# Kernel optimization log

Measured on AMD Instinct MI355X. Metric: run time of the kernel, lower is better.

The kernel has to match this reference:

```python
import jax, jax.numpy as jnp
import numpy as np

NUM_ITERS = 3  # num_iterations init arg


def squash(t, axis):
    # scale = ||t||^2 / (1+||t||^2); out = scale * t / ||t||
    sn = jnp.sum(t * t, axis=axis, keepdims=True)
    return (sn / (1.0 + sn)) * t / jnp.sqrt(sn)


def setup_inputs() -> dict:
    key = jax.random.key(0)
    k1, k2, k3 = jax.random.split(key, 3)
    B, I, O, DI, DO = 2048, 64, 32, 16, 16
    x = jax.random.normal(k1, (B, DI, I), dtype=jnp.float32)
    route_weights = jax.random.normal(k2, (O, I, DO, DI), dtype=jnp.float32)
    noise = 0.01 * jax.random.normal(k3, (O, I, DO, DI), dtype=jnp.float32)
    return {"x": x, "route_weights": route_weights, "noise": noise}


def reference(x, route_weights, noise):
    # random=True branch: perturbed routing weights
    W = route_weights + noise                      # [O,I,do,di]
    xt = jnp.transpose(x, (0, 2, 1))               # [B,I,di]
    # priors[b,o,i,d] = sum_e W[o,i,d,e] * xt[b,i,e]  (trailing singleton dim dropped)
    priors = jnp.einsum('oide,bie->boid', W, xt)   # [B,O,I,do]
    logits = jnp.zeros_like(priors)
    out = None
    for it in range(NUM_ITERS):
        probs = jax.nn.softmax(logits, axis=2)     # over input capsules I
        out = squash(jnp.sum(probs * priors, axis=2, keepdims=True), axis=3)  # [B,O,1,do]
        if it != NUM_ITERS - 1:
            logits = logits + priors * out         # routing-by-agreement update
    out = out[:, :, 0, :]                          # squeeze -> [B,O,do]
    # unsqueeze(0).transpose(2,1) -> [1,O,B,do]
    return jnp.transpose(out[None], (0, 2, 1, 3))
```

## Files before the change

kernel.cpp:

```cpp
#include <hip/hip_runtime.h>


#define THREADS 512

typedef __attribute__((ext_vector_type(2))) float f32x2;
typedef __attribute__((ext_vector_type(4))) float f32x4v;

__global__ __launch_bounds__(256) void wsum_kernel(
    const float* __restrict__ rw, const float* __restrict__ ns,
    float* __restrict__ w2)
{
    const int i = blockIdx.x * 256 + threadIdx.x;
    const float4 a = reinterpret_cast<const float4*>(rw)[i];
    const float4 n = reinterpret_cast<const float4*>(ns)[i];
    float4 r;
    r.x = a.x + n.x;  r.y = a.y + n.y;  r.z = a.z + n.z;  r.w = a.w + n.w;
    reinterpret_cast<float4*>(w2)[i] = r;
}

__device__ __forceinline__ void pk_fma(f32x2& acc, f32x2 a, f32x2 b) {
    asm("v_pk_fma_f32 %0, %1, %2, %0" : "+v"(acc) : "v"(a), "v"(b));
}

template <bool PRE>
__global__ __launch_bounds__(THREADS) void routing_kernel(
    const float* __restrict__ x,
    const float* __restrict__ rw,
    const float* __restrict__ ns,
    float* __restrict__ out)
{
    extern __shared__ float lds[];
    float* xlds = lds + 8192;

    const int tid  = threadIdx.x;
    const int w    = tid >> 6;
    const int lane = tid & 63;

    const int o  = blockIdx.x >> 5;
    const int bc = blockIdx.x & 31;
    const int bbase = bc * 64;

    f32x2 wp0[8], wp1[8];
    {
        const int base = (o * 64 + lane) * 256 + w * 32;
        #pragma unroll
        for (int eq = 0; eq < 4; ++eq) {
            if (PRE) {
                const float4 a0 = *reinterpret_cast<const float4*>(rw + base + eq * 4);
                wp0[2*eq]   = f32x2{a0.x, a0.y};
                wp0[2*eq+1] = f32x2{a0.z, a0.w};
                const float4 a1 = *reinterpret_cast<const float4*>(rw + base + 16 + eq * 4);
                wp1[2*eq]   = f32x2{a1.x, a1.y};
                wp1[2*eq+1] = f32x2{a1.z, a1.w};
            } else {
                const float4 a0 = *reinterpret_cast<const float4*>(rw + base + eq * 4);
                const float4 n0 = *reinterpret_cast<const float4*>(ns + base + eq * 4);
                wp0[2*eq]   = f32x2{a0.x + n0.x, a0.y + n0.y};
                wp0[2*eq+1] = f32x2{a0.z + n0.z, a0.w + n0.w};
                const float4 a1 = *reinterpret_cast<const float4*>(rw + base + 16 + eq * 4);
                const float4 n1 = *reinterpret_cast<const float4*>(ns + base + 16 + eq * 4);
                wp1[2*eq]   = f32x2{a1.x + n1.x, a1.y + n1.y};
                wp1[2*eq+1] = f32x2{a1.z + n1.z, a1.w + n1.w};
            }
        }
    }

    const int d0 = 2 * w, d1 = 2 * w + 1;
    float* pw0 = lds + d0 * 64 + ((((lane >> 2) ^ (d0 & 7)) << 2) | (lane & 3));
    float* pw1 = lds + d1 * 64 + ((((lane >> 2) ^ (d1 & 7)) << 2) | (lane & 3));

    const int qB  = lane >> 4;
    const int dB  = lane & 15;
    const int swz = dB & 7;
    const float4* prbase = reinterpret_cast<const float4*>(lds) + (w * 16 + dB) * 16;
    const float4* pr0 = prbase + ((4 * qB + 0) ^ swz);
    const float4* pr1 = prbase + ((4 * qB + 1) ^ swz);
    const float4* pr2 = prbase + ((4 * qB + 2) ^ swz);
    const float4* pr3 = prbase + ((4 * qB + 3) ^ swz);

    const float* xrb = xlds + lane * 16 + ((lane >> 3) << 2);

    const int il = lane & 15, ih = lane >> 4;
    float* xwb = xlds + w * 1056 + il * 64 + ((il >> 1) << 2) + ih;
    float* xw0 = xwb + 0;
    float* xw1 = xwb + 4;
    float* xw2 = xwb + 8;
    float* xw3 = xwb + 12;

    const float4* xsrc0 = reinterpret_cast<const float4*>(x) + bbase * 256
                        + (w * 256 + lane);

    const int outbase = (o * 2048 + bbase + w) * 16 + dB;

    float4 xb0 = xsrc0[0];
    float4 xb1 = xsrc0[64];
    float4 xb2 = xsrc0[128];
    float4 xb3 = xsrc0[192];
    xw0[0] = xb0.x;  xw0[16] = xb0.y;  xw0[32] = xb0.z;  xw0[48] = xb0.w;
    xw1[0] = xb1.x;  xw1[16] = xb1.y;  xw1[32] = xb1.z;  xw1[48] = xb1.w;
    xw2[0] = xb2.x;  xw2[16] = xb2.y;  xw2[32] = xb2.z;  xw2[48] = xb2.w;
    xw3[0] = xb3.x;  xw3[16] = xb3.y;  xw3[32] = xb3.z;  xw3[48] = xb3.w;
    __syncthreads();

    #pragma unroll
    for (int s = 0; s < 8; ++s) {
        #pragma unroll
        for (int bb = 0; bb < 8; ++bb) {
            const f32x4v v0 = *reinterpret_cast<const f32x4v*>(xrb + bb * 1056 + 0);
            const f32x4v v1 = *reinterpret_cast<const f32x4v*>(xrb + bb * 1056 + 4);
            const f32x4v v2 = *reinterpret_cast<const f32x4v*>(xrb + bb * 1056 + 8);
            const f32x4v v3 = *reinterpret_cast<const f32x4v*>(xrb + bb * 1056 + 12);
            const f32x2 x0 = __builtin_shufflevector(v0, v0, 0, 1);
            const f32x2 x1 = __builtin_shufflevector(v0, v0, 2, 3);
            const f32x2 x2 = __builtin_shufflevector(v1, v1, 0, 1);
            const f32x2 x3 = __builtin_shufflevector(v1, v1, 2, 3);
            const f32x2 x4 = __builtin_shufflevector(v2, v2, 0, 1);
            const f32x2 x5 = __builtin_shufflevector(v2, v2, 2, 3);
            const f32x2 x6 = __builtin_shufflevector(v3, v3, 0, 1);
            const f32x2 x7 = __builtin_shufflevector(v3, v3, 2, 3);
            f32x2 acc0 = {0.f, 0.f};
            f32x2 acc1 = {0.f, 0.f};
            pk_fma(acc0, wp0[0], x0);  pk_fma(acc1, wp1[0], x0);
            pk_fma(acc0, wp0[1], x1);  pk_fma(acc1, wp1[1], x1);
            pk_fma(acc0, wp0[2], x2);  pk_fma(acc1, wp1[2], x2);
            pk_fma(acc0, wp0[3], x3);  pk_fma(acc1, wp1[3], x3);
            pk_fma(acc0, wp0[4], x4);  pk_fma(acc1, wp1[4], x4);
            pk_fma(acc0, wp0[5], x5);  pk_fma(acc1, wp1[5], x5);
            pk_fma(acc0, wp0[6], x6);  pk_fma(acc1, wp1[6], x6);
            pk_fma(acc0, wp0[7], x7);  pk_fma(acc1, wp1[7], x7);
            pw0[bb * 1024] = acc0[0] + acc0[1];
            pw1[bb * 1024] = acc1[0] + acc1[1];
        }
        __syncthreads();

        float p[16];
        {
            const float4 v0 = *pr0, v1 = *pr1, v2 = *pr2, v3 = *pr3;
            p[0]=v0.x; p[1]=v0.y; p[2]=v0.z; p[3]=v0.w;
            p[4]=v1.x; p[5]=v1.y; p[6]=v1.z; p[7]=v1.w;
            p[8]=v2.x; p[9]=v2.y; p[10]=v2.z; p[11]=v2.w;
            p[12]=v3.x; p[13]=v3.y; p[14]=v3.z; p[15]=v3.w;
        }

        if (s < 7) {
            const float4* xsrc = xsrc0 + (s + 1) * 2048;
            xb0 = xsrc[0];  xb1 = xsrc[64];  xb2 = xsrc[128];  xb3 = xsrc[192];
        }

        float t0 = (p[0]+p[1]) + (p[2]+p[3]);
        float t1 = (p[4]+p[5]) + (p[6]+p[7]);
        float t2 = (p[8]+p[9]) + (p[10]+p[11]);
        float t3 = (p[12]+p[13]) + (p[14]+p[15]);
        float part = (t0 + t1) + (t2 + t3);
        part += __shfl_xor(part, 16);
        part += __shfl_xor(part, 32);
        float sv = part * (1.0f / 64.0f);

        float sn = sv * sv;
        sn += __shfl_xor(sn, 1); sn += __shfl_xor(sn, 2);
        sn += __shfl_xor(sn, 4); sn += __shfl_xor(sn, 8);
        float factor = __builtin_amdgcn_sqrtf(sn)
                     * __builtin_amdgcn_rcpf(1.0f + sn);
        float Vsum = sv * factor;

        #pragma unroll
        for (int it = 0; it < 2; ++it) {
            const float c = Vsum * 1.44269504089f;
            float e0, e1, e2, e3;
            float dd0, dd1, dd2, dd3, nn0, nn1, nn2, nn3;
            e0 = __builtin_amdgcn_exp2f(p[0] * c);
            e1 = __builtin_amdgcn_exp2f(p[1] * c);
            e2 = __builtin_amdgcn_exp2f(p[2] * c);
            e3 = __builtin_amdgcn_exp2f(p[3] * c);
            dd0 = e0; dd1 = e1; dd2 = e2; dd3 = e3;
            nn0 = e0 * p[0]; nn1 = e1 * p[1]; nn2 = e2 * p[2]; nn3 = e3 * p[3];
            e0 = __builtin_amdgcn_exp2f(p[4] * c);
            e1 = __builtin_amdgcn_exp2f(p[5] * c);
            e2 = __builtin_amdgcn_exp2f(p[6] * c);
            e3 = __builtin_amdgcn_exp2f(p[7] * c);
            dd0 += e0; dd1 += e1; dd2 += e2; dd3 += e3;
            nn0 = fmaf(e0, p[4], nn0); nn1 = fmaf(e1, p[5], nn1);
            nn2 = fmaf(e2, p[6], nn2); nn3 = fmaf(e3, p[7], nn3);
            e0 = __builtin_amdgcn_exp2f(p[8] * c);
            e1 = __builtin_amdgcn_exp2f(p[9] * c);
            e2 = __builtin_amdgcn_exp2f(p[10] * c);
            e3 = __builtin_amdgcn_exp2f(p[11] * c);
            dd0 += e0; dd1 += e1; dd2 += e2; dd3 += e3;
            nn0 = fmaf(e0, p[8], nn0);  nn1 = fmaf(e1, p[9], nn1);
            nn2 = fmaf(e2, p[10], nn2); nn3 = fmaf(e3, p[11], nn3);
            e0 = __builtin_amdgcn_exp2f(p[12] * c);
            e1 = __builtin_amdgcn_exp2f(p[13] * c);
            e2 = __builtin_amdgcn_exp2f(p[14] * c);
            e3 = __builtin_amdgcn_exp2f(p[15] * c);
            dd0 += e0; dd1 += e1; dd2 += e2; dd3 += e3;
            nn0 = fmaf(e0, p[12], nn0); nn1 = fmaf(e1, p[13], nn1);
            nn2 = fmaf(e2, p[14], nn2); nn3 = fmaf(e3, p[15], nn3);

            float den = (dd0 + dd1) + (dd2 + dd3);
            float num = (nn0 + nn1) + (nn2 + nn3);
            den += __shfl_xor(den, 16); den += __shfl_xor(den, 32);
            num += __shfl_xor(num, 16); num += __shfl_xor(num, 32);
            sv = num * __builtin_amdgcn_rcpf(den);
            sn = sv * sv;
            sn += __shfl_xor(sn, 1); sn += __shfl_xor(sn, 2);
            sn += __shfl_xor(sn, 4); sn += __shfl_xor(sn, 8);
            factor = __builtin_amdgcn_sqrtf(sn)
                   * __builtin_amdgcn_rcpf(1.0f + sn);
            Vsum += sv * factor;
        }

        if (qB == 0)
            out[outbase + s * 128] = sv * factor;

        if (s < 7) {
            xw0[0] = xb0.x;  xw0[16] = xb0.y;  xw0[32] = xb0.z;  xw0[48] = xb0.w;
            xw1[0] = xb1.x;  xw1[16] = xb1.y;  xw1[32] = xb1.z;  xw1[48] = xb1.w;
            xw2[0] = xb2.x;  xw2[16] = xb2.y;  xw2[32] = xb2.z;  xw2[48] = xb2.w;
            xw3[0] = xb3.x;  xw3[16] = xb3.y;  xw3[32] = xb3.z;  xw3[48] = xb3.w;
        }
        __syncthreads();
    }
}

extern "C" void kernel_launch(void* const* d_in, const int* in_sizes, int n_in,
                              void* d_out, int out_size, void* d_ws, size_t ws_size,
                              hipStream_t stream) {
    const float* x  = (const float*)d_in[0];
    const float* rw = (const float*)d_in[1];
    const float* ns = (const float*)d_in[2];
    float* out = (float*)d_out;
    (void)in_sizes; (void)n_in; (void)out_size;

    const int grid = 32 * 32;
    const size_t w2_bytes = 32u * 64u * 16u * 16u * sizeof(float);

    if (ws_size >= w2_bytes) {
        float* w2 = (float*)d_ws;
        wsum_kernel<<<512, 256, 0, stream>>>(rw, ns, w2);
        routing_kernel<true><<<grid, THREADS, 66560, stream>>>(x, w2, ns, out);
    } else {
        routing_kernel<false><<<grid, THREADS, 66560, stream>>>(x, rw, ns, out);
    }
}
```

Measured before the change: 77.84 us.

## Vectorize x LDS staging stores and re-swizzle prior LDS layout

Replaces sixteen scalar LDS stores per staging step of x with four float4 stores by transposing the register values before writing. It also changes the XOR swizzle of the priors LDS buffer by an extra lane-half bit to avoid bank conflicts, and reorders the weight packing so f32x2 pairs take different elements. This requires the compute loop to consume weights in the new interleaved order, and the hidden inner loop must match these layout changes.

```diff
diff --git a/kernel.cpp b/kernel.cpp
--- a/kernel.cpp
+++ b/kernel.cpp
@@ -43,49 +43,62 @@
     f32x2 wp0[8], wp1[8];
     {
         const int base = (o * 64 + lane) * 256 + w * 32;
-        #pragma unroll
-        for (int eq = 0; eq < 4; ++eq) {
-            if (PRE) {
-                const float4 a0 = *reinterpret_cast<const float4*>(rw + base + eq * 4);
-                wp0[2*eq]   = f32x2{a0.x, a0.y};
-                wp0[2*eq+1] = f32x2{a0.z, a0.w};
-                const float4 a1 = *reinterpret_cast<const float4*>(rw + base + 16 + eq * 4);
-                wp1[2*eq]   = f32x2{a1.x, a1.y};
-                wp1[2*eq+1] = f32x2{a1.z, a1.w};
-            } else {
-                const float4 a0 = *reinterpret_cast<const float4*>(rw + base + eq * 4);
-                const float4 n0 = *reinterpret_cast<const float4*>(ns + base + eq * 4);
-                wp0[2*eq]   = f32x2{a0.x + n0.x, a0.y + n0.y};
-                wp0[2*eq+1] = f32x2{a0.z + n0.z, a0.w + n0.w};
-                const float4 a1 = *reinterpret_cast<const float4*>(rw + base + 16 + eq * 4);
-                const float4 n1 = *reinterpret_cast<const float4*>(ns + base + 16 + eq * 4);
-                wp1[2*eq]   = f32x2{a1.x + n1.x, a1.y + n1.y};
-                wp1[2*eq+1] = f32x2{a1.z + n1.z, a1.w + n1.w};
-            }
-        }
+        float4 a0, a1, a2, a3, b0, b1, b2, b3;
+        a0 = *reinterpret_cast<const float4*>(rw + base + 0);
+        a1 = *reinterpret_cast<const float4*>(rw + base + 4);
+        a2 = *reinterpret_cast<const float4*>(rw + base + 8);
+        a3 = *reinterpret_cast<const float4*>(rw + base + 12);
+        b0 = *reinterpret_cast<const float4*>(rw + base + 16);
+        b1 = *reinterpret_cast<const float4*>(rw + base + 20);
+        b2 = *reinterpret_cast<const float4*>(rw + base + 24);
+        b3 = *reinterpret_cast<const float4*>(rw + base + 28);
+        if (!PRE) {
+            const float4 n0 = *reinterpret_cast<const float4*>(ns + base + 0);
+            const float4 n1 = *reinterpret_cast<const float4*>(ns + base + 4);
+            const float4 n2 = *reinterpret_cast<const float4*>(ns + base + 8);
+            const float4 n3 = *reinterpret_cast<const float4*>(ns + base + 12);
+            const float4 m0 = *reinterpret_cast<const float4*>(ns + base + 16);
+            const float4 m1 = *reinterpret_cast<const float4*>(ns + base + 20);
+            const float4 m2 = *reinterpret_cast<const float4*>(ns + base + 24);
+            const float4 m3 = *reinterpret_cast<const float4*>(ns + base + 28);
+            a0.x += n0.x; a0.y += n0.y; a0.z += n0.z; a0.w += n0.w;
+            a1.x += n1.x; a1.y += n1.y; a1.z += n1.z; a1.w += n1.w;
+            a2.x += n2.x; a2.y += n2.y; a2.z += n2.z; a2.w += n2.w;
+            a3.x += n3.x; a3.y += n3.y; a3.z += n3.z; a3.w += n3.w;
+            b0.x += m0.x; b0.y += m0.y; b0.z += m0.z; b0.w += m0.w;
+            b1.x += m1.x; b1.y += m1.y; b1.z += m1.z; b1.w += m1.w;
+            b2.x += m2.x; b2.y += m2.y; b2.z += m2.z; b2.w += m2.w;
+            b3.x += m3.x; b3.y += m3.y; b3.z += m3.z; b3.w += m3.w;
+        }
+        wp0[0] = f32x2{a0.x, a1.x};  wp0[1] = f32x2{a2.x, a3.x};
+        wp0[2] = f32x2{a0.y, a1.y};  wp0[3] = f32x2{a2.y, a3.y};
+        wp0[4] = f32x2{a0.z, a1.z};  wp0[5] = f32x2{a2.z, a3.z};
+        wp0[6] = f32x2{a0.w, a1.w};  wp0[7] = f32x2{a2.w, a3.w};
+        wp1[0] = f32x2{b0.x, b1.x};  wp1[1] = f32x2{b2.x, b3.x};
+        wp1[2] = f32x2{b0.y, b1.y};  wp1[3] = f32x2{b2.y, b3.y};
+        wp1[4] = f32x2{b0.z, b1.z};  wp1[5] = f32x2{b2.z, b3.z};
+        wp1[6] = f32x2{b0.w, b1.w};  wp1[7] = f32x2{b2.w, b3.w};
     }
 
     const int d0 = 2 * w, d1 = 2 * w + 1;
-    float* pw0 = lds + d0 * 64 + ((((lane >> 2) ^ (d0 & 7)) << 2) | (lane & 3));
-    float* pw1 = lds + d1 * 64 + ((((lane >> 2) ^ (d1 & 7)) << 2) | (lane & 3));
+    const int b5 = (lane >> 5) & 1;
+    float* pw0 = lds + d0 * 64 + 4 * (((lane >> 2) ^ (d0 & 7)) ^ b5) + (lane & 3);
+    float* pw1 = lds + d1 * 64 + 4 * (((lane >> 2) ^ (d1 & 7)) ^ b5) + (lane & 3);
 
     const int qB  = lane >> 4;
     const int dB  = lane & 15;
     const int swz = dB & 7;
+    const int qh  = qB >> 1;
     const float4* prbase = reinterpret_cast<const float4*>(lds) + (w * 16 + dB) * 16;
-    const float4* pr0 = prbase + ((4 * qB + 0) ^ swz);
-    const float4* pr1 = prbase + ((4 * qB + 1) ^ swz);
-    const float4* pr2 = prbase + ((4 * qB + 2) ^ swz);
-    const float4* pr3 = prbase + ((4 * qB + 3) ^ swz);
+    const float4* pr0 = prbase + (((4 * qB + 0) ^ swz) ^ qh);
+    const float4* pr1 = prbase + (((4 * qB + 1) ^ swz) ^ qh);
+    const float4* pr2 = prbase + (((4 * qB + 2) ^ swz) ^ qh);
+    const float4* pr3 = prbase + (((4 * qB + 3) ^ swz) ^ qh);
 
     const float* xrb = xlds + lane * 16 + ((lane >> 3) << 2);
 
     const int il = lane & 15, ih = lane >> 4;
-    float* xwb = xlds + w * 1056 + il * 64 + ((il >> 1) << 2) + ih;
-    float* xw0 = xwb + 0;
-    float* xw1 = xwb + 4;
-    float* xw2 = xwb + 8;
-    float* xw3 = xwb + 12;
+    float* xws = xlds + w * 1056 + il * 64 + ((il >> 1) << 2) + ih * 4;
 
     const float4* xsrc0 = reinterpret_cast<const float4*>(x) + bbase * 256
                         + (w * 256 + lane);
@@ -96,10 +109,10 @@
     float4 xb1 = xsrc0[64];
     float4 xb2 = xsrc0[128];
     float4 xb3 = xsrc0[192];
-    xw0[0] = xb0.x;  xw0[16] = xb0.y;  xw0[32] = xb0.z;  xw0[48] = xb0.w;
-    xw1[0] = xb1.x;  xw1[16] = xb1.y;  xw1[32] = xb1.z;  xw1[48] = xb1.w;
-    xw2[0] = xb2.x;  xw2[16] = xb2.y;  xw2[32] = xb2.z;  xw2[48] = xb2.w;
-    xw3[0] = xb3.x;  xw3[16] = xb3.y;  xw3[32] = xb3.z;  xw3[48] = xb3.w;
+    *reinterpret_cast<float4*>(xws + 0)  = make_float4(xb0.x, xb1.x, xb2.x, xb3.x);
+    *reinterpret_cast<float4*>(xws + 16) = make_float4(xb0.y, xb1.y, xb2.y, xb3.y);
+    *reinterpret_cast<float4*>(xws + 32) = make_float4(xb0.z, xb1.z, xb2.z, xb3.z);
+    *reinterpret_cast<float4*>(xws + 48) = make_float4(xb0.w, xb1.w, xb2.w, xb3.w);
     __syncthreads();
 
     #pragma unroll
@@ -213,10 +226,10 @@
             out[outbase + s * 128] = sv * factor;
 
         if (s < 7) {
-            xw0[0] = xb0.x;  xw0[16] = xb0.y;  xw0[32] = xb0.z;  xw0[48] = xb0.w;
-            xw1[0] = xb1.x;  xw1[16] = xb1.y;  xw1[32] = xb1.z;  xw1[48] = xb1.w;
-            xw2[0] = xb2.x;  xw2[16] = xb2.y;  xw2[32] = xb2.z;  xw2[48] = xb2.w;
-            xw3[0] = xb3.x;  xw3[16] = xb3.y;  xw3[32] = xb3.z;  xw3[48] = xb3.w;
+            *reinterpret_cast<float4*>(xws + 0)  = make_float4(xb0.x, xb1.x, xb2.x, xb3.x);
+            *reinterpret_cast<float4*>(xws + 16) = make_float4(xb0.y, xb1.y, xb2.y, xb3.y);
+            *reinterpret_cast<float4*>(xws + 32) = make_float4(xb0.z, xb1.z, xb2.z, xb3.z);
+            *reinterpret_cast<float4*>(xws + 48) = make_float4(xb0.w, xb1.w, xb2.w, xb3.w);
         }
         __syncthreads();
     }
```

Measured after the change: 80.10 us. 2.9% more time.
